# Optimization experiments

Hardware: AMD Instinct MI355X
Metric: run time of the kernel (lower is better)

## Reference

```python
import jax, jax.numpy as jnp
import numpy as np

LOW_RANK = 32      # low_rank_dim
N_CAND = 2048      # n_candidates
CHUNK = 128        # chunk_size
AUX_PCT = 0.2      # Settings.aux_loss_percent


def _normalize(x, eps=1e-12):
    # matches torch.nn.functional.normalize(p=2, dim=-1)
    n = jnp.linalg.norm(x, axis=-1, keepdims=True)
    return x / jnp.maximum(n, eps)


def setup_inputs() -> dict:
    key = jax.random.key(0)
    k1, k2, k3 = jax.random.split(key, 3)
    V, D, B, S = 50257, 1024, 4, 2048
    return {
        "hidden_states": jax.random.normal(k1, (B, S, D), jnp.float32),
        "embedding_weight": jax.random.normal(k2, (V, D), jnp.float32) * 0.02,
        "logit_scale": jnp.asarray(2.6592, jnp.float32),
        "target_ids": jax.random.randint(k3, (B, S), 0, V, dtype=jnp.int32),
    }


def reference(hidden_states, embedding_weight, logit_scale, target_ids):
    d = hidden_states.shape[-1]
    h = hidden_states.reshape(-1, d)            # [T, d]
    t = target_ids.reshape(-1)                  # [T]
    T = h.shape[0]
    n_chunks = T // CHUNK                       # T assumed divisible by CHUNK

    # no_grad low-rank table used only for candidate scan
    w_low_norm = jax.lax.stop_gradient(_normalize(embedding_weight[:, :LOW_RANK]))  # [V, L]
    h_low = _normalize(h[:, :LOW_RANK]).reshape(n_chunks, CHUNK, LOW_RANK)          # [n, C, L]
    h_full = _normalize(h).reshape(n_chunks, CHUNK, d)                              # [n, C, d]
    t_c = t.reshape(n_chunks, CHUNK)

    scale = 100.0 * jax.nn.sigmoid(logit_scale) + 1.0

    # with_batch_mean=True path: one scan per chunk using chunk-mean query (no_grad)
    h_mean = jax.lax.stop_gradient(h_low.mean(axis=1))      # [n, L]
    scan_logits = h_mean @ w_low_norm.T                     # [n, V]
    _, top_idx = jax.lax.top_k(scan_logits, N_CAND)         # [n, K]

    cand = embedding_weight[top_idx]                        # [n, K, d] (gather)
    cand_n = _normalize(cand)
    full_sims = jnp.einsum('ncd,nkd->nck', h_full, cand_n)  # [n, C, K]

    w_low_cand = _normalize(cand[..., :LOW_RANK])           # [n, K, L]
    low_sims = jnp.einsum('ncl,nkl->nck', h_low, w_low_cand)

    tgt_emb = embedding_weight[t_c]                         # [n, C, d]
    tgt_full_sim = jnp.sum(h_full * _normalize(tgt_emb), axis=-1)              # [n, C]
    tgt_low_sim = jnp.sum(h_low * _normalize(tgt_emb[..., :LOW_RANK]), axis=-1)

    is_tgt = top_idx[:, None, :] == t_c[:, :, None]         # [n, C, K]
    neg_inf = jnp.float32(-jnp.inf)

    # cross_entropy with label 0 == logsumexp(logits) - logits[..., 0]
    main_logits = jnp.concatenate(
        [tgt_full_sim[..., None] * scale,
         jnp.where(is_tgt, neg_inf, full_sims * scale)], axis=-1)
    main_loss = jnp.sum(jax.nn.logsumexp(main_logits, axis=-1) - main_logits[..., 0])

    aux_logits = jnp.concatenate(
        [tgt_low_sim[..., None] * scale,
         jnp.where(is_tgt, neg_inf, low_sims * scale)], axis=-1)
    aux_loss = jnp.sum(jax.nn.logsumexp(aux_logits, axis=-1) - aux_logits[..., 0])

    return (main_loss + AUX_PCT * aux_loss) / T
```

## Files before the change

kernel.cpp:

```cpp
#include <hip/hip_runtime.h>
#include <cstdint>
#include <cstddef>

#define V_SIZE 50257
#define V_PAD  50432
#define NV4    (V_PAD/4)
#define NVB    ((V_SIZE + 3) / 4)
#define D_DIM  1024
#define T_TOK  8192
#define NCHUNK 64
#define CCHUNK 128
#define NCAND  2048
#define NTILES 16
#define LOWR   32
#define SDCAP  6144

typedef unsigned int  uint32;
typedef unsigned short u16;
typedef unsigned long long u64;
typedef __attribute__((ext_vector_type(8))) short short8;
typedef __attribute__((ext_vector_type(4))) float f32x4;

__device__ __forceinline__ u16 f2bf(float f){
  uint32 u = __float_as_uint(f);
  return (u16)((u + 0x7FFFu + ((u >> 16) & 1u)) >> 16);
}
__device__ __forceinline__ uint32 key_of(float f){
  uint32 b = __float_as_uint(f);
  return b ^ ((uint32)((int)b >> 31) | 0x80000000u);
}
__device__ __forceinline__ float sigscale(const float* lsc){
  return 100.f / (1.f + __expf(-lsc[0])) + 1.f;
}
__device__ __forceinline__ float wred_sum(float v){
  #pragma unroll
  for (int m = 32; m >= 1; m >>= 1) v += __shfl_xor(v, m, 64);
  return v;
}
__device__ __forceinline__ float wred_max(float v){
  #pragma unroll
  for (int m = 32; m >= 1; m >>= 1) v = fmaxf(v, __shfl_xor(v, m, 64));
  return v;
}
__device__ __forceinline__ void gload_lds16(const void* g, void* l){
  __builtin_amdgcn_global_load_lds(
      (const __attribute__((address_space(1))) uint32*)g,
      (__attribute__((address_space(3))) uint32*)l, 16, 0, 0);
}
__device__ __forceinline__ void load_row16(const float* base, int lane, float* f){
  const float4* s4 = (const float4*)(base + lane * 16);
  float4 t0 = s4[0], t1 = s4[1], t2 = s4[2], t3 = s4[3];
  f[0]=t0.x; f[1]=t0.y; f[2]=t0.z;  f[3]=t0.w;
  f[4]=t1.x; f[5]=t1.y; f[6]=t1.z;  f[7]=t1.w;
  f[8]=t2.x; f[9]=t2.y; f[10]=t2.z; f[11]=t2.w;
  f[12]=t3.x; f[13]=t3.y; f[14]=t3.z; f[15]=t3.w;
}
__device__ __forceinline__ void store_bf16x16(u16* dst_base, int lane, const float* f){
  uint32 pk[8];
  #pragma unroll
  for (int i=0;i<8;++i) pk[i] = (uint32)f2bf(f[2*i]) | ((uint32)f2bf(f[2*i+1]) << 16);
  uint4* d = (uint4*)(dst_base + lane * 16);
  d[0] = make_uint4(pk[0],pk[1],pk[2],pk[3]);
  d[1] = make_uint4(pk[4],pk[5],pk[6],pk[7]);
}

__global__ void __launch_bounds__(256)
prep_kernel(const float* __restrict__ emb, u16* __restrict__ emb16,
            float* __restrict__ invn_f, float* __restrict__ invn_l,
            float* __restrict__ wlow,
            const float* __restrict__ h, u16* __restrict__ h16,
            float* __restrict__ invh_f, float* __restrict__ invh_l,
            float* __restrict__ hpart, float* __restrict__ out)
{
  const int bid = blockIdx.x;
  const int tid = threadIdx.x, lane = tid & 63, wid = tid >> 6;
  if (bid < NVB){
    if (bid == 0 && tid == 0) out[0] = 0.f;
    const int v = bid * 4 + wid;
    if (v >= V_SIZE) return;
    float f[16];
    load_row16(emb + (size_t)v * D_DIM, lane, f);
    float ss = 0.f;
    #pragma unroll
    for (int k=0;k<16;++k) ss += f[k]*f[k];
    float fullss = wred_sum(ss);
    float lowss  = wred_sum(lane < 2 ? ss : 0.f);
    store_bf16x16(emb16 + (size_t)v * D_DIM, lane, f);
    if (lane < 2){
      float4* wp = (float4*)(wlow + (size_t)v * LOWR + lane * 16);
      wp[0] = make_float4(f[0], f[1], f[2],  f[3]);
      wp[1] = make_float4(f[4], f[5], f[6],  f[7]);
      wp[2] = make_float4(f[8], f[9], f[10], f[11]);
      wp[3] = make_float4(f[12],f[13],f[14], f[15]);
    }
    if (lane == 0){
      invn_f[v] = 1.f / fmaxf(sqrtf(fullss), 1e-12f);
      invn_l[v] = 1.f / fmaxf(sqrtf(lowss),  1e-12f);
    }
    return;
  }
  const int bid2 = bid - NVB;
  const int nchunk = bid2 >> 3, sub = bid2 & 7;
  __shared__ float hm[LOWR];
  if (tid < LOWR) hm[tid] = 0.f;
  __syncthreads();
  for (int i = 0; i < 4; ++i){
    const int loc = sub*16 + wid*4 + i;
    const int tok = nchunk * CCHUNK + loc;
    float f[16];
    load_row16(h + (size_t)tok * D_DIM, lane, f);
    float ss = 0.f;
    #pragma unroll
    for (int k=0;k<16;++k) ss += f[k]*f[k];
    float fullss = wred_sum(ss);
    float lowss  = wred_sum(lane < 2 ? ss : 0.f);
    float invf = 1.f / fmaxf(sqrtf(fullss), 1e-12f);
    float invl = 1.f / fmaxf(sqrtf(lowss),  1e-12f);
    store_bf16x16(h16 + (size_t)tok * D_DIM, lane, f);
    if (lane == 0){ invh_f[tok] = invf; invh_l[tok] = invl; }
    if (lane < 2){
      #pragma unroll
      for (int k=0;k<16;++k) atomicAdd(&hm[lane*16 + k], f[k] * invl * (1.f/128.f));
    }
  }
  __syncthreads();
  if (tid < LOWR) hpart[(size_t)(nchunk*8 + sub) * LOWR + tid] = hm[tid];
}

__global__ void __launch_bounds__(256)
scan_kernel(const float* __restrict__ wlow, const float* __restrict__ invn_l,
            const float* __restrict__ hpart, float* __restrict__ scan)
{
  __shared__ float hm[NCHUNK * LOWR];
  for (int i = threadIdx.x; i < NCHUNK * LOWR; i += 256){
    const int nn = i >> 5, l = i & 31;
    float s = 0.f;
    #pragma unroll
    for (int p = 0; p < 8; ++p) s += hpart[(size_t)(nn*8 + p) * LOWR + l];
    hm[i] = s;
  }
  __syncthreads();
  const int v = blockIdx.x * 256 + threadIdx.x;
  if (v >= V_SIZE){
    if (v < V_PAD)
      for (int nn = 0; nn < NCHUNK; ++nn) scan[(size_t)nn * V_PAD + v] = -3.4e38f;
    return;
  }
  float w[LOWR];
  const float4* s4 = (const float4*)(wlow + (size_t)v * LOWR);
  #pragma unroll
  for (int i=0;i<8;++i){
    float4 t = s4[i];
    w[4*i]=t.x; w[4*i+1]=t.y; w[4*i+2]=t.z; w[4*i+3]=t.w;
  }
  const float inv = invn_l[v];
  #pragma unroll
  for (int i=0;i<LOWR;++i) w[i] *= inv;
  for (int nn = 0; nn < NCHUNK; ++nn){
    float d = 0.f;
    #pragma unroll
    for (int l=0;l<LOWR;++l) d += w[l] * hm[nn*LOWR + l];
    scan[(size_t)nn * V_PAD + v] = d;
  }
}

__global__ void __launch_bounds__(1024)
topk_all(const float* __restrict__ scan,
         const float* __restrict__ invn_f, const float* __restrict__ invn_l,
         int* __restrict__ topidx, float* __restrict__ invc_f, float* __restrict__ invc_l)
{
  const int nchunk = blockIdx.x, tid = threadIdx.x, lane = tid & 63;
  __shared__ uint32 h8[8][2048];
  __shared__ int gt_list[2048];
  __shared__ u64 sd_list[SDCAP];
  __shared__ uint32 rh[256];
  __shared__ uint32 n_gt, n_sd, s_tb, s_cgt, s_sel, s_cum, s_pos;
  if (tid == 0){ n_gt = 0; n_sd = 0; s_pos = 0; }
  for (int i = tid; i < 8*2048; i += 1024) (&h8[0][0])[i] = 0;
  __syncthreads();
  const float4* row = (const float4*)(scan + (size_t)nchunk * V_PAD);
  const int cp = (tid >> 6) & 7;
  for (int i = tid; i < NV4; i += 1024){
    float4 x = row[i];
    atomicAdd(&h8[cp][key_of(x.x) >> 21], 1u);
    atomicAdd(&h8[cp][key_of(x.y) >> 21], 1u);
    atomicAdd(&h8[cp][key_of(x.z) >> 21], 1u);
    atomicAdd(&h8[cp][key_of(x.w) >> 21], 1u);
  }
  __syncthreads();
  for (int i = tid; i < 2048; i += 1024){
    uint32 s = h8[0][i];
    #pragma unroll
    for (int c = 1; c < 8; ++c) s += h8[c][i];
    h8[0][i] = s;
  }
  __syncthreads();
  if (tid < 64){
    uint32 c = 0;
    #pragma unroll 8
    for (int k = 0; k < 32; ++k) c += h8[0][lane*32 + k];
    uint32 s = c;
    #pragma unroll
    for (int off = 1; off < 64; off <<= 1){
      uint32 t = __shfl_down(s, off, 64);
      if (lane + off < 64) s += t;
    }
    u64 m1 = __ballot(s >= NCAND);
    const int g = 63 - __builtin_clzll(m1);
    const uint32 cum = (g < 63) ? __shfl(s, g + 1, 64) : 0u;
    uint32 s2 = (lane < 32) ? h8[0][g*32 + lane] : 0u;
    #pragma unroll
    for (int off = 1; off < 32; off <<= 1){
      uint32 t = __shfl_down(s2, off, 64);
      if (lane + off < 32) s2 += t;
    }
    u64 m2 = __ballot((lane < 32) && (cum + s2 >= NCAND));
    const int j = 63 - __builtin_clzll(m2);
    const uint32 cgt = cum + ((j < 31) ? __shfl(s2, j + 1, 64) : 0u);
    if (lane == 0){ s_tb = (uint32)(g*32 + j); s_cgt = cgt; }
  }
  __syncthreads();
  const uint32 tb = s_tb, cgt = s_cgt;
  for (int i = tid; i < NV4; i += 1024){
    float4 x = row[i];
    const int vbase = i * 4;
    float vals[4] = {x.x, x.y, x.z, x.w};
    #pragma unroll
    for (int c = 0; c < 4; ++c){
      uint32 u = key_of(vals[c]);
      uint32 b = u >> 21;
      const int v = vbase + c;
      const bool ok = (v < V_SIZE) && (b >= tb);
      const bool is_gt = ok && (b > tb);
      const bool is_sd = ok && (b == tb);
      const u64 mg = __ballot(is_gt);
      if (mg){
        const int ldr = (int)__builtin_ctzll(mg);
        uint32 base = 0;
        if (lane == ldr) base = atomicAdd(&n_gt, (uint32)__popcll(mg));
        base = __shfl(base, ldr, 64);
        if (is_gt){
          uint32 p = base + (uint32)__popcll(mg & ((1ull << lane) - 1ull));
          if (p < 2048u) gt_list[p] = v;
        }
      }
      const u64 ms = __ballot(is_sd);
      if (ms){
        const int ldr = (int)__builtin_ctzll(ms);
        uint32 base = 0;
        if (lane == ldr) base = atomicAdd(&n_sd, (uint32)__popcll(ms));
        base = __shfl(base, ldr, 64);
        if (is_sd){
          uint32 p = base + (uint32)__popcll(ms & ((1ull << lane) - 1ull));
          if (p < (uint32)SDCAP) sd_list[p] = ((u64)(~u) << 32) | (uint32)v;
        }
      }
    }
  }
  __syncthreads();
  const uint32 ng = n_gt < 2048u ? n_gt : 2048u;
  for (uint32 i = tid; i < ng; i += 1024){
    const int v = gt_list[i];
    const int o = nchunk * NCAND + (int)i;
    topidx[o] = v; invc_f[o] = invn_f[v]; invc_l[o] = invn_l[v];
  }
  const int n = (int)(n_sd < (uint32)SDCAP ? n_sd : (uint32)SDCAP);
  uint32 r = NCAND - cgt; if ((int)r > n) r = (uint32)n;
  u64 pref = sd_list[0] & 0xFF00000000000000ull;
  uint32 rem = r;
  const int bytes6[6] = {6,5,4,2,1,0};
  for (int bi = 0; bi < 6; ++bi){
    const int by = bytes6[bi];
    if (tid < 256) rh[tid] = 0;
    __syncthreads();
    const u64 pmask = (~0ull) << ((by+1)*8);
    for (int i = tid; i < n; i += 1024){
      u64 x = sd_list[i];
      if ((x & pmask) == pref) atomicAdd(&rh[(uint32)(x >> (by*8)) & 255u], 1u);
    }
    __syncthreads();
    if (tid < 64){
      const uint32 b0 = rh[lane*4], b1 = rh[lane*4+1], b2 = rh[lane*4+2], b3 = rh[lane*4+3];
      uint32 ps = b0 + b1 + b2 + b3;
      #pragma unroll
      for (int off = 1; off < 64; off <<= 1){
        uint32 t = __shfl_up(ps, off, 64);
        if (lane >= off) ps += t;
      }
      const u64 mm = __ballot(ps >= rem);
      const int gl = (int)__builtin_ctzll(mm);
      const uint32 before = (gl > 0) ? __shfl(ps, gl-1, 64) : 0u;
      if (lane == gl){
        uint32 cum = before; uint32 bsel = (uint32)gl * 4;
        if (cum + b0 < rem){ cum += b0; bsel++;
          if (cum + b1 < rem){ cum += b1; bsel++;
            if (cum + b2 < rem){ cum += b2; bsel++; } } }
        s_sel = bsel; s_cum = cum;
      }
    }
    __syncthreads();
    pref |= ((u64)s_sel) << (by*8);
    rem -= s_cum;
    __syncthreads();
  }
  for (int i = tid; i < n; i += 1024){
    u64 x = sd_list[i];
    if (x <= pref){
      uint32 p = atomicAdd(&s_pos, 1u);
      const int v = (int)(uint32)x;
      const int o = nchunk * NCAND + (int)(cgt + p);
      topidx[o] = v; invc_f[o] = invn_f[v]; invc_l[o] = invn_l[v];
    }
  }
}

__global__ void __launch_bounds__(256)
gemm_fused(const u16* __restrict__ h16, const u16* __restrict__ emb16,
           const int* __restrict__ topidx,
           const float* __restrict__ invh_f, const float* __restrict__ invc_f,
           const float* __restrict__ invh_l, const float* __restrict__ invc_l,
           const int* __restrict__ tgts, const float* __restrict__ lsc,
           float* __restrict__ pm, float* __restrict__ pa)
{
  constexpr int BK = 64, NSTEP = D_DIM / BK, KK = BK / 32;
  const int id = blockIdx.x;
  const int s_ = id >> 3;
  const int ntile = s_ & 15;
  const int nchunk = ((s_ >> 4) << 3) | (id & 7);
  const int tid = threadIdx.x, lane = tid & 63, wid = tid >> 6;
  const int wm = wid >> 1, wn = wid & 1;
  const int fq = lane >> 4, fr = lane & 15;

  __shared__ u16 As[CCHUNK * BK];
  __shared__ u16 Bs[CCHUNK * BK];
  __shared__ float s_invh[CCHUNK], s_invc[CCHUNK];
  __shared__ float s_invhl[CCHUNK], s_invcl[CCHUNK];
  __shared__ int   s_tgt[CCHUNK], s_idx[CCHUNK];

  if (tid < CCHUNK){
    s_invh[tid]  = invh_f[nchunk * CCHUNK + tid];
    s_invhl[tid] = invh_l[nchunk * CCHUNK + tid];
    s_tgt[tid]   = tgts[nchunk * CCHUNK + tid];
    int o = nchunk * NCAND + ntile * CCHUNK + tid;
    s_idx[tid]   = topidx[o];
    s_invc[tid]  = invc_f[o];
    s_invcl[tid] = invc_l[o];
  }

  const int rl = lane >> 3;
  const int cbyte = ((lane & 7) ^ (rl & 7)) * 16;
  const char* aptr[4];
  const char* bptr[4];
  #pragma unroll
  for (int s = 0; s < 4; ++s){
    int row = wid * 32 + s * 8 + rl;
    aptr[s] = (const char*)h16 + ((size_t)(nchunk * CCHUNK + row)) * (D_DIM * 2) + cbyte;
    int cidx = topidx[nchunk * NCAND + ntile * CCHUNK + row];
    bptr[s] = (const char*)emb16 + (size_t)cidx * (D_DIM * 2) + cbyte;
  }

  f32x4 acc[4][4];
  #pragma unroll
  for (int m=0;m<4;++m)
    #pragma unroll
    for (int q=0;q<4;++q)
      acc[m][q] = (f32x4){0.f,0.f,0.f,0.f};

  for (int st = 0; st < NSTEP; ++st){
    const int koff = st * BK * 2;
    #pragma unroll
    for (int s = 0; s < 4; ++s){
      gload_lds16(aptr[s] + koff, (void*)&As[(wid*32 + s*8) * BK]);
      gload_lds16(bptr[s] + koff, (void*)&Bs[(wid*32 + s*8) * BK]);
    }
    __syncthreads();
    #pragma unroll
    for (int kk = 0; kk < KK; ++kk){
      short8 af[4], bf[4];
      #pragma unroll
      for (int m=0;m<4;++m){
        const int r = wm*64 + m*16 + fr, slot = kk*4 + fq;
        af[m] = *(const short8*)&As[r*BK + ((slot ^ (r & 7)) << 3)];
      }
      #pragma unroll
      for (int q=0;q<4;++q){
        const int r = wn*64 + q*16 + fr, slot = kk*4 + fq;
        bf[q] = *(const short8*)&Bs[r*BK + ((slot ^ (r & 7)) << 3)];
      }
      #pragma unroll
      for (int m=0;m<4;++m)
        #pragma unroll
        for (int q=0;q<4;++q)
          acc[m][q] = __builtin_amdgcn_mfma_f32_16x16x32_bf16(af[m], bf[q], acc[m][q], 0, 0, 0);
    }
    __syncthreads();
  }

  {
    const int rla = lane >> 2;
    const int cba = ((lane & 3) ^ (rla & 3)) * 16;
    #pragma unroll
    for (int s = 0; s < 2; ++s){
      int row = wid * 32 + s * 16 + rla;
      const char* ap = (const char*)h16 + ((size_t)(nchunk * CCHUNK + row)) * (D_DIM * 2) + cba;
      int cidx = topidx[nchunk * NCAND + ntile * CCHUNK + row];
      const char* bp = (const char*)emb16 + (size_t)cidx * (D_DIM * 2) + cba;
      gload_lds16(ap, (void*)&As[(wid*32 + s*16) * 32]);
      gload_lds16(bp, (void*)&Bs[(wid*32 + s*16) * 32]);
    }
  }

  const float scale = sigscale(lsc);
  const float NEG = -__builtin_huge_valf();

  #pragma unroll
  for (int m=0;m<4;++m){
    #pragma unroll
    for (int j=0;j<4;++j){
      const int c = wm*64 + m*16 + fq*4 + j;
      const float ihs = s_invh[c] * scale;
      const int tg = s_tgt[c];
      float vals[4];
      #pragma unroll
      for (int q=0;q<4;++q){
        const int kl = wn*64 + q*16 + fr;
        float lg = acc[m][q][j] * ihs * s_invc[kl];
        vals[q] = (s_idx[kl] == tg) ? NEG : lg;
      }
      float lmax = fmaxf(fmaxf(vals[0], vals[1]), fmaxf(vals[2], vals[3]));
      #pragma unroll
      for (int ms=1; ms<16; ms<<=1) lmax = fmaxf(lmax, __shfl_xor(lmax, ms, 64));
      float se = 0.f;
      #pragma unroll
      for (int q=0;q<4;++q) se += __expf(vals[q] - lmax);
      #pragma unroll
      for (int ms=1; ms<16; ms<<=1) se += __shfl_xor(se, ms, 64);
      if (fr == 0){
        size_t pos = ((size_t)((nchunk*NTILES + ntile)*2 + wn) * CCHUNK + c) * 2;
        pm[pos]   = lmax;
        pm[pos+1] = se;
      }
    }
  }

  __syncthreads();

  f32x4 acc2[4][4];
  {
    short8 afa[4], bfa[4];
    #pragma unroll
    for (int m=0;m<4;++m){
      const int r = wm*64 + m*16 + fr;
      afa[m] = *(const short8*)&As[r*32 + ((fq ^ (r & 3)) << 3)];
    }
    #pragma unroll
    for (int q=0;q<4;++q){
      const int r = wn*64 + q*16 + fr;
      bfa[q] = *(const short8*)&Bs[r*32 + ((fq ^ (r & 3)) << 3)];
    }
    #pragma unroll
    for (int m=0;m<4;++m)
      #pragma unroll
      for (int q=0;q<4;++q)
        acc2[m][q] = __builtin_amdgcn_mfma_f32_16x16x32_bf16(
            afa[m], bfa[q], (f32x4){0.f,0.f,0.f,0.f}, 0, 0, 0);
  }

  #pragma unroll
  for (int m=0;m<4;++m){
    #pragma unroll
    for (int j=0;j<4;++j){
      const int c = wm*64 + m*16 + fq*4 + j;
      const float ihs = s_invhl[c] * scale;
      const int tg = s_tgt[c];
      float vals[4];
      #pragma unroll
      for (int q=0;q<4;++q){
        const int kl = wn*64 + q*16 + fr;
        float lg = acc2[m][q][j] * ihs * s_invcl[kl];
        vals[q] = (s_idx[kl] == tg) ? NEG : lg;
      }
      float lmax = fmaxf(fmaxf(vals[0], vals[1]), fmaxf(vals[2], vals[3]));
      #pragma unroll
      for (int ms=1; ms<16; ms<<=1) lmax = fmaxf(lmax, __shfl_xor(lmax, ms, 64));
      float se = 0.f;
      #pragma unroll
      for (int q=0;q<4;++q) se += __expf(vals[q] - lmax);
      #pragma unroll
      for (int ms=1; ms<16; ms<<=1) se += __shfl_xor(se, ms, 64);
      if (fr == 0){
        size_t pos = ((size_t)((nchunk*NTILES + ntile)*2 + wn) * CCHUNK + c) * 2;
        pa[pos]   = lmax;
        pa[pos+1] = se;
      }
    }
  }
}

__global__ void __launch_bounds__(256)
merge_loss(const u16* __restrict__ h16, const u16* __restrict__ emb16,
           const int* __restrict__ tgts,
           const float* __restrict__ invh_f, const float* __restrict__ invh_l,
           const float* __restrict__ invn_f, const float* __restrict__ invn_l,
           const float* __restrict__ pm, const float* __restrict__ pa,
           const float* __restrict__ lsc, float* __restrict__ out)
{
  const int nchunk = blockIdx.x >> 2, quarter = blockIdx.x & 3;
  const int tid = threadIdx.x, lane = tid & 63, wid = tid >> 6;
  const float scale = sigscale(lsc);
  const float NEG = -__builtin_huge_valf();
  float wacc = 0.f;
  for (int i = 0; i < 8; ++i){
    const int loc = quarter*32 + wid*8 + i;
    const int tok = nchunk * CCHUNK + loc;
    const int t = tgts[tok];
    float part = 0.f;
    {
      const uint4* hp = (const uint4*)(h16 + (size_t)tok * D_DIM) + lane*2;
      const uint4* ep = (const uint4*)(emb16 + (size_t)t * D_DIM) + lane*2;
      uint4 hx = hp[0], hy = hp[1], ex = ep[0], ey = ep[1];
      uint32 hu[8] = {hx.x,hx.y,hx.z,hx.w,hy.x,hy.y,hy.z,hy.w};
      uint32 eu[8] = {ex.x,ex.y,ex.z,ex.w,ey.x,ey.y,ey.z,ey.w};
      #pragma unroll
      for (int k=0;k<8;++k){
        float h0 = __uint_as_float(hu[k] << 16);
        float h1 = __uint_as_float(hu[k] & 0xFFFF0000u);
        float e0 = __uint_as_float(eu[k] << 16);
        float e1 = __uint_as_float(eu[k] & 0xFFFF0000u);
        part += h0*e0 + h1*e1;
      }
    }
    float dfull = wred_sum(part);
    float dlow  = wred_sum(lane < 2 ? part : 0.f);
    float tful = dfull * invh_f[tok] * invn_f[t] * scale;
    float tlow = dlow  * invh_l[tok] * invn_l[t] * scale;

    float mi = NEG, si = 0.f, mia = NEG, sia = 0.f;
    if (lane < 32){
      size_t q = ((size_t)(nchunk*32 + lane) * CCHUNK + loc) * 2;
      mi  = pm[q]; si  = pm[q+1];
      mia = pa[q]; sia = pa[q+1];
    }
    float M  = wred_max(mi);
    float S  = wred_sum(lane < 32 ? si * __expf(mi - M) : 0.f);
    float M2 = fmaxf(M, tful);
    float lmain = __logf(S * __expf(M - M2) + __expf(tful - M2)) + M2 - tful;
    float Ma  = wred_max(mia);
    float Sa  = wred_sum(lane < 32 ? sia * __expf(mia - Ma) : 0.f);
    float M2a = fmaxf(Ma, tlow);
    float laux = __logf(Sa * __expf(Ma - M2a) + __expf(tlow - M2a)) + M2a - tlow;
    wacc += lmain + 0.2f * laux;
  }
  __shared__ float ws4[4];
  if (lane == 0) ws4[wid] = wacc;
  __syncthreads();
  if (tid == 0) atomicAdd(out, (ws4[0]+ws4[1]+ws4[2]+ws4[3]) * (1.f / (float)T_TOK));
}

extern "C" void kernel_launch(void* const* d_in, const int* in_sizes, int n_in,
                              void* d_out, int out_size, void* d_ws, size_t ws_size,
                              hipStream_t stream)
{
  (void)in_sizes; (void)n_in; (void)out_size; (void)ws_size;
  const float* h   = (const float*)d_in[0];
  const float* emb = (const float*)d_in[1];
  const float* lsc = (const float*)d_in[2];
  const int*   tgt = (const int*)d_in[3];
  float* out = (float*)d_out;

  uint8_t* p = (uint8_t*)d_ws;
  auto carve = [&](size_t n)->uint8_t*{
    uint8_t* r = p; p += (n + 255) & ~(size_t)255; return r;
  };
  u16*   emb16  = (u16*)  carve((size_t)V_SIZE * D_DIM * 2);
  float* invn_f = (float*)carve((size_t)V_SIZE * 4);
  float* invn_l = (float*)carve((size_t)V_SIZE * 4);
  float* wlow   = (float*)carve((size_t)V_SIZE * LOWR * 4);
  u16*   h16    = (u16*)  carve((size_t)T_TOK * D_DIM * 2);
  float* invh_f = (float*)carve((size_t)T_TOK * 4);
  float* invh_l = (float*)carve((size_t)T_TOK * 4);
  float* hpart  = (float*)carve((size_t)NCHUNK * 8 * LOWR * 4);
  float* scan   = (float*)carve((size_t)NCHUNK * V_PAD * 4);
  int*   topidx = (int*)  carve((size_t)NCHUNK * NCAND * 4);
  float* invc_f = (float*)carve((size_t)NCHUNK * NCAND * 4);
  float* invc_l = (float*)carve((size_t)NCHUNK * NCAND * 4);
  float* pm     = (float*)carve((size_t)NCHUNK * 32 * CCHUNK * 2 * 4);
  float* pa     = (float*)carve((size_t)NCHUNK * 32 * CCHUNK * 2 * 4);

  prep_kernel<<<dim3(NVB + NCHUNK*8), dim3(256), 0, stream>>>(
      emb, emb16, invn_f, invn_l, wlow, h, h16, invh_f, invh_l, hpart, out);
  scan_kernel<<<dim3(V_PAD / 256), dim3(256), 0, stream>>>(wlow, invn_l, hpart, scan);
  topk_all<<<dim3(NCHUNK), dim3(1024), 0, stream>>>(
      scan, invn_f, invn_l, topidx, invc_f, invc_l);
  gemm_fused<<<dim3(NTILES * NCHUNK), dim3(256), 0, stream>>>(
      h16, emb16, topidx, invh_f, invc_f, invh_l, invc_l, tgt, lsc, pm, pa);
  merge_loss<<<dim3(NCHUNK * 4), dim3(256), 0, stream>>>(
      h16, emb16, tgt, invh_f, invh_l, invn_f, invn_l, pm, pa, lsc, out);
}
```

Baseline: 212.6 us.

## Switch full-dim candidate GEMM to FP8 MFMA with separate bf16 low-rank copies

Stores the embedding table and hidden states as fp8, with the embedding pre-scaled by 32 to limit underflow, and runs the full-dimension candidate similarity GEMM with fp8 MFMA at half the bytes per K step. Small separate bf16 copies of the first 32 columns keep the low-rank aux similarities in bf16. The target-similarity kernel now reads the original fp32 inputs. This halves the prep-kernel write traffic and the GEMM gather traffic, at the cost of lower precision in the main-loss logits.

After: 192.1 us. 9.7% less time.

```diff
diff --git a/kernel.cpp b/kernel.cpp
--- a/kernel.cpp
+++ b/kernel.cpp
@@ -14,9 +14,11 @@
 #define NTILES 16
 #define LOWR   32
 #define SDCAP  6144
+#define ESCALE 32.0f
 
 typedef unsigned int  uint32;
 typedef unsigned short u16;
+typedef unsigned char u8;
 typedef unsigned long long u64;
 typedef __attribute__((ext_vector_type(8))) short short8;
 typedef __attribute__((ext_vector_type(4))) float f32x4;
@@ -63,12 +65,27 @@
   d[0] = make_uint4(pk[0],pk[1],pk[2],pk[3]);
   d[1] = make_uint4(pk[4],pk[5],pk[6],pk[7]);
 }
+__device__ __forceinline__ void store_fp8x16(u8* dst_base, int lane, const float* f, float sc){
+  uint32 pk[4];
+  #pragma unroll
+  for (int i=0;i<4;++i){
+    int w = __builtin_amdgcn_cvt_pk_fp8_f32(f[4*i]*sc,   f[4*i+1]*sc, 0, false);
+    w     = __builtin_amdgcn_cvt_pk_fp8_f32(f[4*i+2]*sc, f[4*i+3]*sc, w, true);
+    pk[i] = (uint32)w;
+  }
+  *(uint4*)(dst_base + lane * 16) = make_uint4(pk[0],pk[1],pk[2],pk[3]);
+}
+__device__ __forceinline__ int a8(int r, int slot8){
+  return r*64 + ((((slot8>>1) ^ (r&3))) << 4) + ((slot8&1) << 3);
+}
 
 __global__ void __launch_bounds__(256)
-prep_kernel(const float* __restrict__ emb, u16* __restrict__ emb16,
+prep_kernel(const float* __restrict__ emb, u8* __restrict__ emb8,
+            u16* __restrict__ elow16,
             float* __restrict__ invn_f, float* __restrict__ invn_l,
             float* __restrict__ wlow,
-            const float* __restrict__ h, u16* __restrict__ h16,
+            const float* __restrict__ h, u8* __restrict__ h8,
+            u16* __restrict__ hlow16,
             float* __restrict__ invh_f, float* __restrict__ invh_l,
             float* __restrict__ hpart, float* __restrict__ out)
 {
@@ -85,8 +102,9 @@
     for (int k=0;k<16;++k) ss += f[k]*f[k];
     float fullss = wred_sum(ss);
     float lowss  = wred_sum(lane < 2 ? ss : 0.f);
-    store_bf16x16(emb16 + (size_t)v * D_DIM, lane, f);
+    store_fp8x16(emb8 + (size_t)v * D_DIM, lane, f, ESCALE);
     if (lane < 2){
+      store_bf16x16(elow16 + (size_t)v * LOWR, lane, f);
       float4* wp = (float4*)(wlow + (size_t)v * LOWR + lane * 16);
       wp[0] = make_float4(f[0], f[1], f[2],  f[3]);
       wp[1] = make_float4(f[4], f[5], f[6],  f[7]);
@@ -116,7 +134,8 @@
     float lowss  = wred_sum(lane < 2 ? ss : 0.f);
     float invf = 1.f / fmaxf(sqrtf(fullss), 1e-12f);
     float invl = 1.f / fmaxf(sqrtf(lowss),  1e-12f);
-    store_bf16x16(h16 + (size_t)tok * D_DIM, lane, f);
+    store_fp8x16(h8 + (size_t)tok * D_DIM, lane, f, 1.0f);
+    if (lane < 2) store_bf16x16(hlow16 + (size_t)tok * LOWR, lane, f);
     if (lane == 0){ invh_f[tok] = invf; invh_l[tok] = invl; }
     if (lane < 2){
       #pragma unroll
@@ -170,35 +189,35 @@
          int* __restrict__ topidx, float* __restrict__ invc_f, float* __restrict__ invc_l)
 {
   const int nchunk = blockIdx.x, tid = threadIdx.x, lane = tid & 63;
-  __shared__ uint32 h8[8][2048];
+  __shared__ uint32 h8v[8][2048];
   __shared__ int gt_list[2048];
   __shared__ u64 sd_list[SDCAP];
   __shared__ uint32 rh[256];
   __shared__ uint32 n_gt, n_sd, s_tb, s_cgt, s_sel, s_cum, s_pos;
   if (tid == 0){ n_gt = 0; n_sd = 0; s_pos = 0; }
-  for (int i = tid; i < 8*2048; i += 1024) (&h8[0][0])[i] = 0;
+  for (int i = tid; i < 8*2048; i += 1024) (&h8v[0][0])[i] = 0;
   __syncthreads();
   const float4* row = (const float4*)(scan + (size_t)nchunk * V_PAD);
   const int cp = (tid >> 6) & 7;
   for (int i = tid; i < NV4; i += 1024){
     float4 x = row[i];
-    atomicAdd(&h8[cp][key_of(x.x) >> 21], 1u);
-    atomicAdd(&h8[cp][key_of(x.y) >> 21], 1u);
-    atomicAdd(&h8[cp][key_of(x.z) >> 21], 1u);
-    atomicAdd(&h8[cp][key_of(x.w) >> 21], 1u);
+    atomicAdd(&h8v[cp][key_of(x.x) >> 21], 1u);
+    atomicAdd(&h8v[cp][key_of(x.y) >> 21], 1u);
+    atomicAdd(&h8v[cp][key_of(x.z) >> 21], 1u);
+    atomicAdd(&h8v[cp][key_of(x.w) >> 21], 1u);
   }
   __syncthreads();
   for (int i = tid; i < 2048; i += 1024){
-    uint32 s = h8[0][i];
-    #pragma unroll
-    for (int c = 1; c < 8; ++c) s += h8[c][i];
-    h8[0][i] = s;
+    uint32 s = h8v[0][i];
+    #pragma unroll
+    for (int c = 1; c < 8; ++c) s += h8v[c][i];
+    h8v[0][i] = s;
   }
   __syncthreads();
   if (tid < 64){
     uint32 c = 0;
     #pragma unroll 8
-    for (int k = 0; k < 32; ++k) c += h8[0][lane*32 + k];
+    for (int k = 0; k < 32; ++k) c += h8v[0][lane*32 + k];
     uint32 s = c;
     #pragma unroll
     for (int off = 1; off < 64; off <<= 1){
@@ -208,7 +227,7 @@
     u64 m1 = __ballot(s >= NCAND);
     const int g = 63 - __builtin_clzll(m1);
     const uint32 cum = (g < 63) ? __shfl(s, g + 1, 64) : 0u;
-    uint32 s2 = (lane < 32) ? h8[0][g*32 + lane] : 0u;
+    uint32 s2 = (lane < 32) ? h8v[0][g*32 + lane] : 0u;
     #pragma unroll
     for (int off = 1; off < 32; off <<= 1){
       uint32 t = __shfl_down(s2, off, 64);
@@ -315,14 +334,15 @@
 }
 
 __global__ void __launch_bounds__(256)
-gemm_fused(const u16* __restrict__ h16, const u16* __restrict__ emb16,
+gemm_fused(const u8* __restrict__ h8, const u8* __restrict__ emb8,
+           const u16* __restrict__ hlow16, const u16* __restrict__ elow16,
            const int* __restrict__ topidx,
            const float* __restrict__ invh_f, const float* __restrict__ invc_f,
            const float* __restrict__ invh_l, const float* __restrict__ invc_l,
            const int* __restrict__ tgts, const float* __restrict__ lsc,
            float* __restrict__ pm, float* __restrict__ pa)
 {
-  constexpr int BK = 64, NSTEP = D_DIM / BK, KK = BK / 32;
+  constexpr int NSTEP = 16;
   const int id = blockIdx.x;
   const int s_ = id >> 3;
   const int ntile = s_ & 15;
@@ -331,8 +351,8 @@
   const int wm = wid >> 1, wn = wid & 1;
   const int fq = lane >> 4, fr = lane & 15;
 
-  __shared__ u16 As[CCHUNK * BK];
-  __shared__ u16 Bs[CCHUNK * BK];
+  __shared__ u8 As[CCHUNK * 64];
+  __shared__ u8 Bs[CCHUNK * 64];
   __shared__ float s_invh[CCHUNK], s_invc[CCHUNK];
   __shared__ float s_invhl[CCHUNK], s_invcl[CCHUNK];
   __shared__ int   s_tgt[CCHUNK], s_idx[CCHUNK];
@@ -347,16 +367,16 @@
     s_invcl[tid] = invc_l[o];
   }
 
-  const int rl = lane >> 3;
-  const int cbyte = ((lane & 7) ^ (rl & 7)) * 16;
-  const char* aptr[4];
-  const char* bptr[4];
-  #pragma unroll
-  for (int s = 0; s < 4; ++s){
-    int row = wid * 32 + s * 8 + rl;
-    aptr[s] = (const char*)h16 + ((size_t)(nchunk * CCHUNK + row)) * (D_DIM * 2) + cbyte;
+  const int rl = lane >> 2;
+  const int cbyte = ((lane & 3) ^ (rl & 3)) * 16;
+  const char* aptr[2];
+  const char* bptr[2];
+  #pragma unroll
+  for (int s = 0; s < 2; ++s){
+    int row = wid * 32 + s * 16 + rl;
+    aptr[s] = (const char*)h8 + ((size_t)(nchunk * CCHUNK + row)) * D_DIM + cbyte;
     int cidx = topidx[nchunk * NCAND + ntile * CCHUNK + row];
-    bptr[s] = (const char*)emb16 + (size_t)cidx * (D_DIM * 2) + cbyte;
+    bptr[s] = (const char*)emb8 + (size_t)cidx * D_DIM + cbyte;
   }
 
   f32x4 acc[4][4];
@@ -367,50 +387,45 @@
       acc[m][q] = (f32x4){0.f,0.f,0.f,0.f};
 
   for (int st = 0; st < NSTEP; ++st){
-    const int koff = st * BK * 2;
-    #pragma unroll
-    for (int s = 0; s < 4; ++s){
-      gload_lds16(aptr[s] + koff, (void*)&As[(wid*32 + s*8) * BK]);
-      gload_lds16(bptr[s] + koff, (void*)&Bs[(wid*32 + s*8) * BK]);
+    const int koff = st * 64;
+    #pragma unroll
+    for (int s = 0; s < 2; ++s){
+      gload_lds16(aptr[s] + koff, (void*)&As[(wid*32 + s*16) * 64]);
+      gload_lds16(bptr[s] + koff, (void*)&Bs[(wid*32 + s*16) * 64]);
     }
     __syncthreads();
     #pragma unroll
-    for (int kk = 0; kk < KK; ++kk){
-      short8 af[4], bf[4];
-      #pragma unroll
-      for (int m=0;m<4;++m){
-        const int r = wm*64 + m*16 + fr, slot = kk*4 + fq;
-        af[m] = *(const short8*)&As[r*BK + ((slot ^ (r & 7)) << 3)];
-      }
-      #pragma unroll
-      for (int q=0;q<4;++q){
-        const int r = wn*64 + q*16 + fr, slot = kk*4 + fq;
-        bf[q] = *(const short8*)&Bs[r*BK + ((slot ^ (r & 7)) << 3)];
-      }
+    for (int kk = 0; kk < 2; ++kk){
+      long af[4], bf[4];
+      #pragma unroll
+      for (int m=0;m<4;++m)
+        af[m] = *(const long*)&As[a8(wm*64 + m*16 + fr, kk*4 + fq)];
+      #pragma unroll
+      for (int q=0;q<4;++q)
+        bf[q] = *(const long*)&Bs[a8(wn*64 + q*16 + fr, kk*4 + fq)];
       #pragma unroll
       for (int m=0;m<4;++m)
         #pragma unroll
         for (int q=0;q<4;++q)
-          acc[m][q] = __builtin_amdgcn_mfma_f32_16x16x32_bf16(af[m], bf[q], acc[m][q], 0, 0, 0);
+          acc[m][q] = __builtin_amdgcn_mfma_f32_16x16x32_fp8_fp8(af[m], bf[q], acc[m][q], 0, 0, 0);
     }
     __syncthreads();
   }
 
   {
-    const int rla = lane >> 2;
-    const int cba = ((lane & 3) ^ (rla & 3)) * 16;
     #pragma unroll
     for (int s = 0; s < 2; ++s){
-      int row = wid * 32 + s * 16 + rla;
-      const char* ap = (const char*)h16 + ((size_t)(nchunk * CCHUNK + row)) * (D_DIM * 2) + cba;
+      int row = wid * 32 + s * 16 + rl;
+      const char* ap = (const char*)hlow16 + ((size_t)(nchunk * CCHUNK + row)) * (LOWR*2) + cbyte;
       int cidx = topidx[nchunk * NCAND + ntile * CCHUNK + row];
-      const char* bp = (const char*)emb16 + (size_t)cidx * (D_DIM * 2) + cba;
-      gload_lds16(ap, (void*)&As[(wid*32 + s*16) * 32]);
-      gload_lds16(bp, (void*)&Bs[(wid*32 + s*16) * 32]);
+      const char* bp = (const char*)elow16 + (size_t)cidx * (LOWR*2) + cbyte;
+      gload_lds16(ap, (void*)&As[(wid*32 + s*16) * 64]);
+      gload_lds16(bp, (void*)&Bs[(wid*32 + s*16) * 64]);
     }
   }
 
   const float scale = sigscale(lsc);
+  const float scm = scale * (1.0f / ESCALE);
   const float NEG = -__builtin_huge_valf();
 
   #pragma unroll
@@ -418,7 +433,7 @@
     #pragma unroll
     for (int j=0;j<4;++j){
       const int c = wm*64 + m*16 + fq*4 + j;
-      const float ihs = s_invh[c] * scale;
+      const float ihs = s_invh[c] * scm;
       const int tg = s_tgt[c];
       float vals[4];
       #pragma unroll
@@ -451,12 +466,12 @@
     #pragma unroll
     for (int m=0;m<4;++m){
       const int r = wm*64 + m*16 + fr;
-      afa[m] = *(const short8*)&As[r*32 + ((fq ^ (r & 3)) << 3)];
+      afa[m] = *(const short8*)&As[r*64 + ((fq ^ (r & 3)) << 4)];
     }
     #pragma unroll
     for (int q=0;q<4;++q){
       const int r = wn*64 + q*16 + fr;
-      bfa[q] = *(const short8*)&Bs[r*32 + ((fq ^ (r & 3)) << 3)];
+      bfa[q] = *(const short8*)&Bs[r*64 + ((fq ^ (r & 3)) << 4)];
     }
     #pragma unroll
     for (int m=0;m<4;++m)
@@ -498,7 +513,7 @@
 }
 
 __global__ void __launch_bounds__(256)
-merge_loss(const u16* __restrict__ h16, const u16* __restrict__ emb16,
+merge_loss(const float* __restrict__ h, const float* __restrict__ emb,
            const int* __restrict__ tgts,
            const float* __restrict__ invh_f, const float* __restrict__ invh_l,
            const float* __restrict__ invn_f, const float* __restrict__ invn_l,
@@ -514,22 +529,12 @@
     const int loc = quarter*32 + wid*8 + i;
     const int tok = nchunk * CCHUNK + loc;
     const int t = tgts[tok];
+    float hf[16], ef[16];
+    load_row16(h + (size_t)tok * D_DIM, lane, hf);
+    load_row16(emb + (size_t)t * D_DIM, lane, ef);
     float part = 0.f;
-    {
-      const uint4* hp = (const uint4*)(h16 + (size_t)tok * D_DIM) + lane*2;
-      const uint4* ep = (const uint4*)(emb16 + (size_t)t * D_DIM) + lane*2;
-      uint4 hx = hp[0], hy = hp[1], ex = ep[0], ey = ep[1];
-      uint32 hu[8] = {hx.x,hx.y,hx.z,hx.w,hy.x,hy.y,hy.z,hy.w};
-      uint32 eu[8] = {ex.x,ex.y,ex.z,ex.w,ey.x,ey.y,ey.z,ey.w};
-      #pragma unroll
-      for (int k=0;k<8;++k){
-        float h0 = __uint_as_float(hu[k] << 16);
-        float h1 = __uint_as_float(hu[k] & 0xFFFF0000u);
-        float e0 = __uint_as_float(eu[k] << 16);
-        float e1 = __uint_as_float(eu[k] & 0xFFFF0000u);
-        part += h0*e0 + h1*e1;
-      }
-    }
+    #pragma unroll
+    for (int k=0;k<16;++k) part += hf[k]*ef[k];
     float dfull = wred_sum(part);
     float dlow  = wred_sum(lane < 2 ? part : 0.f);
     float tful = dfull * invh_f[tok] * invn_f[t] * scale;
@@ -572,11 +577,13 @@
   auto carve = [&](size_t n)->uint8_t*{
     uint8_t* r = p; p += (n + 255) & ~(size_t)255; return r;
   };
-  u16*   emb16  = (u16*)  carve((size_t)V_SIZE * D_DIM * 2);
+  u8*    emb8   = (u8*)   carve((size_t)V_SIZE * D_DIM);
+  u16*   elow16 = (u16*)  carve((size_t)V_SIZE * LOWR * 2);
   float* invn_f = (float*)carve((size_t)V_SIZE * 4);
   float* invn_l = (float*)carve((size_t)V_SIZE * 4);
   float* wlow   = (float*)carve((size_t)V_SIZE * LOWR * 4);
-  u16*   h16    = (u16*)  carve((size_t)T_TOK * D_DIM * 2);
+  u8*    h8     = (u8*)   carve((size_t)T_TOK * D_DIM);
+  u16*   hlow16 = (u16*)  carve((size_t)T_TOK * LOWR * 2);
   float* invh_f = (float*)carve((size_t)T_TOK * 4);
   float* invh_l = (float*)carve((size_t)T_TOK * 4);
   float* hpart  = (float*)carve((size_t)NCHUNK * 8 * LOWR * 4);
@@ -588,12 +595,12 @@
   float* pa     = (float*)carve((size_t)NCHUNK * 32 * CCHUNK * 2 * 4);
 
   prep_kernel<<<dim3(NVB + NCHUNK*8), dim3(256), 0, stream>>>(
-      emb, emb16, invn_f, invn_l, wlow, h, h16, invh_f, invh_l, hpart, out);
+      emb, emb8, elow16, invn_f, invn_l, wlow, h, h8, hlow16, invh_f, invh_l, hpart, out);
   scan_kernel<<<dim3(V_PAD / 256), dim3(256), 0, stream>>>(wlow, invn_l, hpart, scan);
   topk_all<<<dim3(NCHUNK), dim3(1024), 0, stream>>>(
       scan, invn_f, invn_l, topidx, invc_f, invc_l);
   gemm_fused<<<dim3(NTILES * NCHUNK), dim3(256), 0, stream>>>(
-      h16, emb16, topidx, invh_f, invc_f, invh_l, invc_l, tgt, lsc, pm, pa);
+      h8, emb8, hlow16, elow16, topidx, invh_f, invc_f, invh_l, invc_l, tgt, lsc, pm, pa);
   merge_loss<<<dim3(NCHUNK * 4), dim3(256), 0, stream>>>(
-      h16, emb16, tgt, invh_f, invh_l, invn_f, invn_l, pm, pa, lsc, out);
-}
+      h, emb, tgt, invh_f, invh_l, invn_f, invn_l, pm, pa, lsc, out);
+}
```
